# Optimization experiments

Measured on AMD Instinct MI355X. Metric: run time of the kernel, lower is better.

The kernel has to match this reference:

```python
import jax, jax.numpy as jnp
import numpy as np

DIM = 1024
SEQ = 2048
HID = 128
HEADS = 8
DECAY_CONST = SEQ // 512  # 4


def setup_inputs() -> dict:
    key = jax.random.key(0)
    ks = jax.random.split(key, 8)
    x = jax.random.normal(ks[0], (8, DIM, SEQ), dtype=jnp.float32)
    # per-head input projections: Linear(dim, hidden_dim)
    proj_w = jax.random.normal(ks[1], (HEADS, HID, DIM), dtype=jnp.float32) / np.sqrt(DIM)
    proj_b = jax.random.normal(ks[2], (HEADS, HID), dtype=jnp.float32) * 0.01
    # mixer params: weight (seq,), bias (seq,), decay_value scalar per head
    mix_w = jax.random.normal(ks[3], (HEADS, SEQ), dtype=jnp.float32)
    mix_b = jnp.zeros((HEADS, SEQ), dtype=jnp.float32)
    decay_v = jnp.ones((HEADS,), dtype=jnp.float32)
    # output projection Linear(dim, dim)
    out_w = jax.random.normal(ks[4], (DIM, DIM), dtype=jnp.float32) / np.sqrt(DIM)
    out_b = jax.random.normal(ks[5], (DIM,), dtype=jnp.float32) * 0.01
    return {"x": x, "proj_w": proj_w, "proj_b": proj_b, "mix_w": mix_w,
            "mix_b": mix_b, "decay_v": decay_v, "out_w": out_w, "out_b": out_b}


def _decay_matrices(mix_w, decay_v):
    """Build per-head upper-triangular decayed matrices M[h] (S,S).
    First HEADS//2 heads: ColRepeat (value v[j] on column j);
    last HEADS//2 heads: RowRepeat (value v[i] on row i).
    Entry (i,j) for j>=i is v * clip(d,0.9,1)**((j-i)/DECAY_CONST)."""
    S = mix_w.shape[1]
    H2 = HEADS // 2
    i = jnp.arange(S)[:, None]
    j = jnp.arange(S)[None, :]
    mask = j >= i                                  # (S,S)
    expo = jnp.where(mask, (j - i) / DECAY_CONST, 0.0).astype(jnp.float32)
    d = jnp.clip(decay_v, 0.9, 1.0)                # (H,)
    dpow = d[:, None, None] ** expo[None]          # (H,S,S)
    col_v = jnp.broadcast_to(mix_w[:H2, None, :], (H2, S, S))   # v[j]
    row_v = jnp.broadcast_to(mix_w[H2:, :, None], (HEADS - H2, S, S))  # v[i]
    vmat = jnp.concatenate([col_v, row_v], axis=0)  # (H,S,S)
    return jnp.where(mask[None], vmat * dpow, 0.0)


def reference(x, proj_w, proj_b, mix_w, mix_b, decay_v, out_w, out_b):
    # x: (B, E=dim, T=seq)
    x_bte = jnp.transpose(x, (0, 2, 1))                       # (B,T,E)
    proj = jnp.einsum('bte,hde->bhtd', x_bte, proj_w) + proj_b[None, :, None, :]  # (B,H,T,D)
    M = _decay_matrices(mix_w, decay_v)                        # (H,S,S)
    # mixer: out[t'] = sum_t proj[t] * M[t, t'] ; bias is added per-time-step
    mixed = jnp.einsum('bhtd,hts->bhsd', proj, M) + mix_b[None, :, :, None]  # (B,H,S,D)
    B, H, S, D = mixed.shape
    hidden = jnp.transpose(mixed, (0, 2, 1, 3)).reshape(B, S, H * D)  # concat heads
    out = hidden @ out_w.T + out_b                             # (B,S,dim)
    return jnp.transpose(out, (0, 2, 1))                       # (B,dim,S)
```

## Files before the change

kernel.cpp:

```cpp
#include <hip/hip_runtime.h>

#define DIM 1024
#define SEQ 2048
#define HID 128
#define HEADS 8
#define DECAYC 4
#define CHUNK 32
#define NCH (SEQ / CHUNK)
#define BK 64
#define NT (DIM / BK)

typedef __bf16 bf16x8 __attribute__((ext_vector_type(8)));
typedef float f32x4 __attribute__((ext_vector_type(4)));
typedef unsigned short u16x4 __attribute__((ext_vector_type(4)));

__device__ __forceinline__ unsigned short f2bf(float f) {
  union { float f; unsigned u; } v; v.f = f;
  unsigned r = v.u + 0x7fffu + ((v.u >> 16) & 1u);
  return (unsigned short)(r >> 16);
}
__device__ __forceinline__ float bf2f(unsigned short u) {
  union { unsigned u; float f; } v; v.u = ((unsigned)u) << 16;
  return v.f;
}

typedef __attribute__((address_space(1))) const unsigned int* g_u32p;
typedef __attribute__((address_space(3))) unsigned int* l_u32p;

__device__ __forceinline__ void async_ld16(const unsigned short* g, unsigned short* l) {
  __builtin_amdgcn_global_load_lds((g_u32p)g, (l_u32p)l, 16, 0, 0);
}

__global__ void convertk(const float* __restrict__ in, unsigned short* __restrict__ out, int n) {
  int i = blockIdx.x * 256 + threadIdx.x;
  if (i < n) out[i] = f2bf(in[i]);
}

__global__ __launch_bounds__(256) void transpose_x(const float* __restrict__ x,
                                                   unsigned short* __restrict__ xT) {
  __shared__ float tile[64][65];
  const int b = blockIdx.z;
  const int e0 = blockIdx.x * 64;
  const int t0 = blockIdx.y * 64;
  const int tr = threadIdx.x >> 6;
  const int tc = threadIdx.x & 63;
  const float* xp = x + ((size_t)b * DIM + e0) * SEQ + t0;
#pragma unroll
  for (int i = 0; i < 16; ++i) {
    int e = i * 4 + tr;
    tile[e][tc] = xp[(size_t)e * SEQ + tc];
  }
  __syncthreads();
  unsigned short* op = xT + ((size_t)b * SEQ + t0) * DIM + e0;
#pragma unroll
  for (int i = 0; i < 16; ++i) {
    int t = i * 4 + tr;
    op[(size_t)t * DIM + tc] = f2bf(tile[tc][t]);
  }
}

template <int C_BF16, int BIAS_ROW, int MODE>
__global__ __launch_bounds__(512, 2) void gemm256(const unsigned short* __restrict__ A,
                                                  const unsigned short* __restrict__ B,
                                                  void* __restrict__ Cv,
                                                  const float* __restrict__ bias,
                                                  int ldc, long sB, long sC) {
  __shared__ unsigned short lds[65536];

  int m0, n0, z;
  if constexpr (MODE == 1) {
    m0 = (blockIdx.x >> 2) * 256;
    n0 = (blockIdx.x & 3) * 256;
    z = 0;
  } else {
    z = blockIdx.x >> 5;
    m0 = ((blockIdx.x >> 3) & 3) * 256;
    n0 = (blockIdx.x & 7) * 256;
  }
  B += (size_t)sB * z;

  const int tid = threadIdx.x;
  const int lane = tid & 63;
  const int w = tid >> 6;
  const int wm = w >> 2;
  const int wn = w & 3;

  const unsigned short* sp[2][2][2];
#pragma unroll
  for (int j = 0; j < 2; ++j) {
    int c = (w * 2 + j) * 1024 + lane * 16;
    int cs = c ^ (((c >> 7) & 3) << 4);
    int row = cs >> 6;
    int colel = (cs & 63) >> 1;
#pragma unroll
    for (int kh = 0; kh < 2; ++kh) {
      sp[0][kh][j] = A + (size_t)(m0 + row) * DIM + kh * 32 + colel;
      sp[1][kh][j] = B + (size_t)(n0 + row) * DIM + kh * 32 + colel;
    }
  }

  const int r15 = lane & 15;
  const int hi = lane >> 4;
  const int rsw = ((r15 >> 1) & 3) << 4;
  int aoff[8][2], boff[4][2];
#pragma unroll
  for (int fi = 0; fi < 8; ++fi) {
    int byte = ((wm * 128 + fi * 16 + r15) * 64 + hi * 16) ^ rsw;
#pragma unroll
    for (int ks = 0; ks < 2; ++ks) aoff[fi][ks] = ks * 8192 + (byte >> 1);
  }
#pragma unroll
  for (int fj = 0; fj < 4; ++fj) {
    int byte = ((wn * 64 + fj * 16 + r15) * 64 + hi * 16) ^ rsw;
#pragma unroll
    for (int ks = 0; ks < 2; ++ks) boff[fj][ks] = 16384 + ks * 8192 + (byte >> 1);
  }

  f32x4 acc[8][4] = {};

#define STG(dd, op, kh, tgt)                                                    \
  if ((tgt) < NT) {                                                             \
    unsigned short* dst_ = (unsigned short*)lds + (dd) * 32768 + (op) * 16384 + \
                           (kh) * 8192 + w * 1024;                              \
    async_ld16(sp[op][kh][0] + (tgt) * BK, dst_);                               \
    async_ld16(sp[op][kh][1] + (tgt) * BK, dst_ + 512);                         \
  }

#define PHASE(H_, KS_, MIDBAR, STAGE_STMT)                                      \
  {                                                                             \
    bf16x8 af[4], bfr[4];                                                       \
    _Pragma("unroll") for (int i = 0; i < 4; ++i)                               \
        af[i] = *(const bf16x8*)&lb[aoff[(H_) * 4 + i][KS_]];                   \
    _Pragma("unroll") for (int j = 0; j < 4; ++j)                               \
        bfr[j] = *(const bf16x8*)&lb[boff[j][KS_]];                             \
    STAGE_STMT;                                                                 \
    if (MIDBAR) __builtin_amdgcn_s_barrier();                                   \
    asm volatile("s_waitcnt lgkmcnt(0)" ::: "memory");                          \
    __builtin_amdgcn_sched_barrier(0);                                          \
    __builtin_amdgcn_s_setprio(1);                                              \
    _Pragma("unroll") for (int i = 0; i < 4; ++i)                               \
      _Pragma("unroll") for (int j = 0; j < 4; ++j)                             \
        acc[(H_) * 4 + i][j] = __builtin_amdgcn_mfma_f32_16x16x32_bf16(         \
            af[i], bfr[j], acc[(H_) * 4 + i][j], 0, 0, 0);                      \
    __builtin_amdgcn_s_setprio(0);                                              \
    __builtin_amdgcn_s_barrier();                                               \
  }

  STG(0, 0, 0, 0); STG(0, 1, 0, 0); STG(0, 0, 1, 0); STG(0, 1, 1, 0);
  STG(1, 0, 0, 1); STG(1, 1, 0, 1);

#pragma unroll
  for (int t = 0; t < NT; ++t) {
    const int d = t & 1;
    const unsigned short* lb = (const unsigned short*)lds + d * 32768;
    if (t == NT - 1) {
      asm volatile("s_waitcnt vmcnt(0)" ::: "memory");
    } else {
      asm volatile("s_waitcnt vmcnt(4)" ::: "memory");
    }
    __builtin_amdgcn_s_barrier();
    PHASE(0, 0, 0, STG(d ^ 1, 0, 1, t + 1));
    PHASE(1, 0, 1, STG(d ^ 1, 1, 1, t + 1));
    PHASE(0, 1, 1, STG(d, 0, 0, t + 2));
    PHASE(1, 1, 1, STG(d, 1, 0, t + 2));
  }
#undef PHASE
#undef STG

  const int or0 = hi * 4;
#pragma unroll
  for (int fi = 0; fi < 8; ++fi) {
#pragma unroll
    for (int fj = 0; fj < 4; ++fj) {
      const int col = n0 + wn * 64 + fj * 16 + r15;
      const int rowb = m0 + wm * 128 + fi * 16 + or0;
      float cb = BIAS_ROW ? 0.0f : bias[col];
#pragma unroll
      for (int q = 0; q < 4; ++q) {
        const int row = rowb + q;
        float v = acc[fi][fj][q] + (BIAS_ROW ? bias[row] : cb);
        if constexpr (C_BF16) {
          ((unsigned short*)Cv)[(size_t)sC * z + (size_t)row * ldc + col] = f2bf(v);
        } else {
          ((float*)Cv)[(size_t)sC * z + (size_t)row * ldc + col] = v;
        }
      }
    }
  }
}

__global__ __launch_bounds__(256) void scan_carry(const unsigned short* __restrict__ proj,
                                                  float* __restrict__ carry,
                                                  const float* __restrict__ mix_w,
                                                  const float* __restrict__ decay_v) {
  const int b = blockIdx.x >> 6;
  const int c = blockIdx.x & (NCH - 1);
  const int n0 = threadIdx.x * 4;
  const int h = n0 >> 7;
  const float d = fminf(fmaxf(decay_v[h], 0.9f), 1.0f);
  const float r = powf(d, 1.0f / (float)DECAYC);
  const bool colrep = h < (HEADS / 2);
  const u16x4* p = (const u16x4*)(proj + ((size_t)(b * SEQ + c * CHUNK)) * DIM + n0);
  const float* mw = mix_w + h * SEQ + c * CHUNK;
  float s0 = 0.f, s1 = 0.f, s2 = 0.f, s3 = 0.f;
#pragma unroll 8
  for (int t = 0; t < CHUNK; ++t) {
    u16x4 v = p[t * (DIM / 4)];
    float wi = colrep ? 1.0f : mw[t];
    s0 = s0 * r + bf2f(v[0]) * wi;
    s1 = s1 * r + bf2f(v[1]) * wi;
    s2 = s2 * r + bf2f(v[2]) * wi;
    s3 = s3 * r + bf2f(v[3]) * wi;
  }
  f32x4 out = {s0, s1, s2, s3};
  *(f32x4*)(carry + ((size_t)(b * NCH + c)) * DIM + n0) = out;
}

__global__ __launch_bounds__(256) void scan_prefix(float* __restrict__ carry,
                                                   const float* __restrict__ decay_v) {
  const int idx = blockIdx.x * 256 + threadIdx.x;
  const int b = idx >> 10;
  const int n = idx & 1023;
  const int h = n >> 7;
  const float d = fminf(fmaxf(decay_v[h], 0.9f), 1.0f);
  const float r = powf(d, 1.0f / (float)DECAYC);
  const float rL = powf(r, (float)CHUNK);
  float P = 0.0f;
  for (int c = 0; c < NCH; ++c) {
    float* p = carry + ((size_t)(b * NCH + c)) * DIM + n;
    float cc = *p;
    *p = P;
    P = rL * P + cc;
  }
}

__global__ __launch_bounds__(256) void scan_apply(const unsigned short* __restrict__ proj,
                                                  unsigned short* __restrict__ hidden,
                                                  const float* __restrict__ carry,
                                                  const float* __restrict__ mix_w,
                                                  const float* __restrict__ mix_b,
                                                  const float* __restrict__ decay_v) {
  const int b = blockIdx.x >> 6;
  const int c = blockIdx.x & (NCH - 1);
  const int n0 = threadIdx.x * 4;
  const int h = n0 >> 7;
  const float d = fminf(fmaxf(decay_v[h], 0.9f), 1.0f);
  const float r = powf(d, 1.0f / (float)DECAYC);
  const bool colrep = h < (HEADS / 2);
  const size_t base = ((size_t)(b * SEQ + c * CHUNK)) * DIM + n0;
  const u16x4* p = (const u16x4*)(proj + base);
  u16x4* o = (u16x4*)(hidden + base);
  const float* mw = mix_w + h * SEQ + c * CHUNK;
  const float* mb = mix_b + h * SEQ + c * CHUNK;
  f32x4 ci = *(const f32x4*)(carry + ((size_t)(b * NCH + c)) * DIM + n0);
  float s0 = ci[0], s1 = ci[1], s2 = ci[2], s3 = ci[3];
#pragma unroll 8
  for (int t = 0; t < CHUNK; ++t) {
    u16x4 v = p[t * (DIM / 4)];
    float wv = mw[t];
    float wi = colrep ? 1.0f : wv;
    float wo = colrep ? wv : 1.0f;
    float bb = mb[t];
    s0 = s0 * r + bf2f(v[0]) * wi;
    s1 = s1 * r + bf2f(v[1]) * wi;
    s2 = s2 * r + bf2f(v[2]) * wi;
    s3 = s3 * r + bf2f(v[3]) * wi;
    u16x4 ov;
    ov[0] = f2bf(s0 * wo + bb);
    ov[1] = f2bf(s1 * wo + bb);
    ov[2] = f2bf(s2 * wo + bb);
    ov[3] = f2bf(s3 * wo + bb);
    o[t * (DIM / 4)] = ov;
  }
}

extern "C" void kernel_launch(void* const* d_in, const int* in_sizes, int n_in,
                              void* d_out, int out_size, void* d_ws, size_t ws_size,
                              hipStream_t stream) {
  const float* x = (const float*)d_in[0];
  const float* proj_w = (const float*)d_in[1];
  const float* proj_b = (const float*)d_in[2];
  const float* mix_w = (const float*)d_in[3];
  const float* mix_b = (const float*)d_in[4];
  const float* decay_v = (const float*)d_in[5];
  const float* out_w = (const float*)d_in[6];
  const float* out_b = (const float*)d_in[7];

  char* ws = (char*)d_ws;
  unsigned short* xT = (unsigned short*)ws;
  unsigned short* proj = (unsigned short*)(ws + 33554432);
  unsigned short* W1 = (unsigned short*)(ws + 67108864);
  unsigned short* W2 = (unsigned short*)(ws + 69206016);
  unsigned short* hidden = xT;
  float* carryf = (float*)(ws + 67108864);

  const int NW = DIM * DIM;
  convertk<<<dim3((NW + 255) / 256), 256, 0, stream>>>(proj_w, W1, NW);
  convertk<<<dim3((NW + 255) / 256), 256, 0, stream>>>(out_w, W2, NW);
  transpose_x<<<dim3(16, 32, 8), 256, 0, stream>>>(x, xT);

  gemm256<1, 0, 1><<<dim3(256), 512, 0, stream>>>(xT, W1, proj, proj_b, DIM, 0L, 0L);

  scan_carry<<<dim3(8 * NCH), 256, 0, stream>>>(proj, carryf, mix_w, decay_v);
  scan_prefix<<<dim3(8192 / 256), 256, 0, stream>>>(carryf, decay_v);
  scan_apply<<<dim3(8 * NCH), 256, 0, stream>>>(proj, hidden, carryf, mix_w, mix_b, decay_v);

  gemm256<0, 1, 2><<<dim3(256), 512, 0, stream>>>(W2, hidden, d_out, out_b, SEQ,
                                                  (long)SEQ * DIM, (long)DIM * SEQ);
}
```

Measured before the change: 129.5 us.

## Fuse weight conversions, vectorize transpose stores, fold scan prefix, new 256x128 output GEMM

Merges the two weight-conversion kernels into one launch and vectorizes the bf16 stores in the x transpose. Removes the serial scan_prefix kernel: each scan_apply block now recomputes its own chunk prefix from the carries, which saves a launch but adds redundant work for later chunks. Replaces the output GEMM with a new 256x128-tile kernel with a smaller LDS footprint and 512 blocks, aiming for more blocks per CU. The new GEMM uses a simpler double-buffered pipeline with full waits every K-step, which may hide latency less well than the original.

```diff
diff --git a/kernel.cpp b/kernel.cpp
--- a/kernel.cpp
+++ b/kernel.cpp
@@ -31,9 +31,14 @@
   __builtin_amdgcn_global_load_lds((g_u32p)g, (l_u32p)l, 16, 0, 0);
 }
 
-__global__ void convertk(const float* __restrict__ in, unsigned short* __restrict__ out, int n) {
+__global__ void convertk2(const float* __restrict__ in0, unsigned short* __restrict__ out0,
+                          const float* __restrict__ in1, unsigned short* __restrict__ out1,
+                          int n) {
   int i = blockIdx.x * 256 + threadIdx.x;
-  if (i < n) out[i] = f2bf(in[i]);
+  if (i < n) {
+    out0[i] = f2bf(in0[i]);
+    out1[i] = f2bf(in1[i]);
+  }
 }
 
 __global__ __launch_bounds__(256) void transpose_x(const float* __restrict__ x,
@@ -52,10 +57,17 @@
   }
   __syncthreads();
   unsigned short* op = xT + ((size_t)b * SEQ + t0) * DIM + e0;
-#pragma unroll
-  for (int i = 0; i < 16; ++i) {
-    int t = i * 4 + tr;
-    op[(size_t)t * DIM + tc] = f2bf(tile[tc][t]);
+  const int tq = threadIdx.x >> 4;
+  const int e4 = (threadIdx.x & 15) * 4;
+#pragma unroll
+  for (int i = 0; i < 4; ++i) {
+    int t = i * 16 + tq;
+    u16x4 ov;
+    ov[0] = f2bf(tile[e4 + 0][t]);
+    ov[1] = f2bf(tile[e4 + 1][t]);
+    ov[2] = f2bf(tile[e4 + 2][t]);
+    ov[3] = f2bf(tile[e4 + 3][t]);
+    *(u16x4*)&op[(size_t)t * DIM + e4] = ov;
   }
 }
 
@@ -174,6 +186,118 @@
     for (int fj = 0; fj < 4; ++fj) {
       const int col = n0 + wn * 64 + fj * 16 + r15;
       const int rowb = m0 + wm * 128 + fi * 16 + or0;
+      float cb = BIAS_ROW ? 0.0f : bias[col];
+#pragma unroll
+      for (int q = 0; q < 4; ++q) {
+        const int row = rowb + q;
+        float v = acc[fi][fj][q] + (BIAS_ROW ? bias[row] : cb);
+        if constexpr (C_BF16) {
+          ((unsigned short*)Cv)[(size_t)sC * z + (size_t)row * ldc + col] = f2bf(v);
+        } else {
+          ((float*)Cv)[(size_t)sC * z + (size_t)row * ldc + col] = v;
+        }
+      }
+    }
+  }
+}
+
+template <int C_BF16, int BIAS_ROW, int MODE>
+__global__ __launch_bounds__(512, 4) void gemm128n(const unsigned short* __restrict__ A,
+                                                   const unsigned short* __restrict__ B,
+                                                   void* __restrict__ Cv,
+                                                   const float* __restrict__ bias,
+                                                   int ldc, long sB, long sC) {
+  __shared__ unsigned short lds[24576];
+
+  int m0, n0, z;
+  if constexpr (MODE == 1) {
+    m0 = (blockIdx.x >> 3) * 256;
+    n0 = (blockIdx.x & 7) * 128;
+    z = 0;
+  } else {
+    z = blockIdx.x >> 6;
+    m0 = ((blockIdx.x >> 4) & 3) * 256;
+    n0 = (blockIdx.x & 15) * 128;
+  }
+  B += (size_t)sB * z;
+
+  const int tid = threadIdx.x;
+  const int lane = tid & 63;
+  const int w = tid >> 6;
+  const int wm = w >> 2;
+  const int wn = w & 3;
+
+  int c0 = tid * 16;
+  int c1 = 8192 + tid * 16;
+  int c2 = tid * 16;
+  int cs0 = c0 ^ (((c0 >> 7) & 3) << 4);
+  int cs1 = c1 ^ (((c1 >> 7) & 3) << 4);
+  int cs2 = c2 ^ (((c2 >> 7) & 3) << 4);
+  const unsigned short* srcA0 = A + (size_t)(m0 + (cs0 >> 6)) * DIM + ((cs0 & 63) >> 1);
+  const unsigned short* srcA1 = A + (size_t)(m0 + (cs1 >> 6)) * DIM + ((cs1 & 63) >> 1);
+  const unsigned short* srcB0 = B + (size_t)(n0 + (cs2 >> 6)) * DIM + ((cs2 & 63) >> 1);
+
+  const int r15 = lane & 15;
+  const int hi = lane >> 4;
+  const int rsw = ((r15 >> 1) & 3) << 4;
+  const int abase = ((((wm * 128 + r15) * 64) + hi * 16) ^ rsw) >> 1;
+  const int bbase = 8192 + (((((wn * 32 + r15) * 64) + hi * 16) ^ rsw) >> 1);
+
+  f32x4 acc[8][2] = {};
+
+#define STG2(dd, k)                                                \
+  {                                                                \
+    unsigned short* bb_ = (unsigned short*)lds + (dd) * 12288;     \
+    async_ld16(srcA0 + (k), bb_ + tid * 8);                        \
+    async_ld16(srcA1 + (k), bb_ + 4096 + tid * 8);                 \
+    async_ld16(srcB0 + (k), bb_ + 8192 + tid * 8);                 \
+  }
+
+  STG2(0, 0);
+  asm volatile("s_waitcnt vmcnt(0)" ::: "memory");
+  __builtin_amdgcn_s_barrier();
+
+#pragma unroll 2
+  for (int t = 0; t < 32; ++t) {
+    const int d = t & 1;
+    const unsigned short* lb = (const unsigned short*)lds + d * 12288;
+    if (t < 31) STG2(d ^ 1, (t + 1) * 32);
+    bf16x8 bf0 = *(const bf16x8*)&lb[bbase];
+    bf16x8 bf1 = *(const bf16x8*)&lb[bbase + 512];
+    bf16x8 af[4];
+#pragma unroll
+    for (int fi = 0; fi < 4; ++fi) af[fi] = *(const bf16x8*)&lb[abase + fi * 512];
+    asm volatile("s_waitcnt lgkmcnt(0)" ::: "memory");
+    __builtin_amdgcn_sched_barrier(0);
+    __builtin_amdgcn_s_setprio(1);
+#pragma unroll
+    for (int fi = 0; fi < 4; ++fi) {
+      acc[fi][0] = __builtin_amdgcn_mfma_f32_16x16x32_bf16(af[fi], bf0, acc[fi][0], 0, 0, 0);
+      acc[fi][1] = __builtin_amdgcn_mfma_f32_16x16x32_bf16(af[fi], bf1, acc[fi][1], 0, 0, 0);
+    }
+    __builtin_amdgcn_s_setprio(0);
+#pragma unroll
+    for (int fi = 0; fi < 4; ++fi) af[fi] = *(const bf16x8*)&lb[abase + (4 + fi) * 512];
+    asm volatile("s_waitcnt lgkmcnt(0)" ::: "memory");
+    __builtin_amdgcn_sched_barrier(0);
+    __builtin_amdgcn_s_setprio(1);
+#pragma unroll
+    for (int fi = 0; fi < 4; ++fi) {
+      acc[4 + fi][0] = __builtin_amdgcn_mfma_f32_16x16x32_bf16(af[fi], bf0, acc[4 + fi][0], 0, 0, 0);
+      acc[4 + fi][1] = __builtin_amdgcn_mfma_f32_16x16x32_bf16(af[fi], bf1, acc[4 + fi][1], 0, 0, 0);
+    }
+    __builtin_amdgcn_s_setprio(0);
+    asm volatile("s_waitcnt vmcnt(0)" ::: "memory");
+    __builtin_amdgcn_s_barrier();
+  }
+#undef STG2
+
+#pragma unroll
+  for (int fi = 0; fi < 8; ++fi) {
+#pragma unroll
+    for (int fj = 0; fj < 2; ++fj) {
+      const int col = n0 + wn * 32 + fj * 16 + r15;
+      const int rowb = m0 + wm * 128 + fi * 16 + hi * 4;
       float cb = BIAS_ROW ? 0.0f : bias[col];
 #pragma unroll
       for (int q = 0; q < 4; ++q) {
@@ -216,24 +340,6 @@
   *(f32x4*)(carry + ((size_t)(b * NCH + c)) * DIM + n0) = out;
 }
 
-__global__ __launch_bounds__(256) void scan_prefix(float* __restrict__ carry,
-                                                   const float* __restrict__ decay_v) {
-  const int idx = blockIdx.x * 256 + threadIdx.x;
-  const int b = idx >> 10;
-  const int n = idx & 1023;
-  const int h = n >> 7;
-  const float d = fminf(fmaxf(decay_v[h], 0.9f), 1.0f);
-  const float r = powf(d, 1.0f / (float)DECAYC);
-  const float rL = powf(r, (float)CHUNK);
-  float P = 0.0f;
-  for (int c = 0; c < NCH; ++c) {
-    float* p = carry + ((size_t)(b * NCH + c)) * DIM + n;
-    float cc = *p;
-    *p = P;
-    P = rL * P + cc;
-  }
-}
-
 __global__ __launch_bounds__(256) void scan_apply(const unsigned short* __restrict__ proj,
                                                   unsigned short* __restrict__ hidden,
                                                   const float* __restrict__ carry,
@@ -246,14 +352,19 @@
   const int h = n0 >> 7;
   const float d = fminf(fmaxf(decay_v[h], 0.9f), 1.0f);
   const float r = powf(d, 1.0f / (float)DECAYC);
+  const float rL = powf(r, (float)CHUNK);
   const bool colrep = h < (HEADS / 2);
+  f32x4 P = {0.f, 0.f, 0.f, 0.f};
+  for (int j = 0; j < c; ++j) {
+    f32x4 cj = *(const f32x4*)(carry + ((size_t)(b * NCH + j)) * DIM + n0);
+    P = P * rL + cj;
+  }
   const size_t base = ((size_t)(b * SEQ + c * CHUNK)) * DIM + n0;
   const u16x4* p = (const u16x4*)(proj + base);
   u16x4* o = (u16x4*)(hidden + base);
   const float* mw = mix_w + h * SEQ + c * CHUNK;
   const float* mb = mix_b + h * SEQ + c * CHUNK;
-  f32x4 ci = *(const f32x4*)(carry + ((size_t)(b * NCH + c)) * DIM + n0);
-  float s0 = ci[0], s1 = ci[1], s2 = ci[2], s3 = ci[3];
+  float s0 = P[0], s1 = P[1], s2 = P[2], s3 = P[3];
 #pragma unroll 8
   for (int t = 0; t < CHUNK; ++t) {
     u16x4 v = p[t * (DIM / 4)];
@@ -295,16 +406,14 @@
   float* carryf = (float*)(ws + 67108864);
 
   const int NW = DIM * DIM;
-  convertk<<<dim3((NW + 255) / 256), 256, 0, stream>>>(proj_w, W1, NW);
-  convertk<<<dim3((NW + 255) / 256), 256, 0, stream>>>(out_w, W2, NW);
+  convertk2<<<dim3((NW + 255) / 256), 256, 0, stream>>>(proj_w, W1, out_w, W2, NW);
   transpose_x<<<dim3(16, 32, 8), 256, 0, stream>>>(x, xT);
 
   gemm256<1, 0, 1><<<dim3(256), 512, 0, stream>>>(xT, W1, proj, proj_b, DIM, 0L, 0L);
 
   scan_carry<<<dim3(8 * NCH), 256, 0, stream>>>(proj, carryf, mix_w, decay_v);
-  scan_prefix<<<dim3(8192 / 256), 256, 0, stream>>>(carryf, decay_v);
   scan_apply<<<dim3(8 * NCH), 256, 0, stream>>>(proj, hidden, carryf, mix_w, mix_b, decay_v);
 
-  gemm256<0, 1, 2><<<dim3(256), 512, 0, stream>>>(W2, hidden, d_out, out_b, SEQ,
-                                                  (long)SEQ * DIM, (long)DIM * SEQ);
-}
+  gemm128n<0, 1, 2><<<dim3(512), 512, 0, stream>>>(W2, hidden, d_out, out_b, SEQ,
+                                                   (long)SEQ * DIM, (long)DIM * SEQ);
+}
```

Result: slower. 137.9 us (+6.5%).
